# Performance work log

Measured on AMD Instinct MI355X. Metric: run time of the kernel, lower is better.

## Reference

```python
import jax, jax.numpy as jnp
import numpy as np

N_FEATURES = 64
KERNEL = 3
PAD = KERNEL // 2


def setup_inputs() -> dict:
    key = jax.random.key(0)
    ks = jax.random.split(key, 6)
    B, C, D, H, W = 2, N_FEATURES, 64, 64, 64
    Q = jax.random.normal(ks[0], (B, C, D, H, W), dtype=jnp.float32)
    K = jax.random.normal(ks[1], (B, C, D, H, W), dtype=jnp.float32)
    V = jax.random.normal(ks[2], (B, C, D, H, W), dtype=jnp.float32)
    # learned params: positional embedding (torch.randn init) and 1x1x1 conv
    pos_emb = jax.random.normal(ks[3], (C, KERNEL, KERNEL, KERNEL), dtype=jnp.float32)
    fan_in = C  # 1x1x1 conv fan-in
    bound = 1.0 / np.sqrt(fan_in)
    W_out = jax.random.uniform(ks[4], (C, C), minval=-bound, maxval=bound, dtype=jnp.float32)
    b_out = jax.random.uniform(ks[5], (C,), minval=-bound, maxval=bound, dtype=jnp.float32)
    return {"Q": Q, "K": K, "V": V, "pos_emb": pos_emb, "W_out": W_out, "b_out": b_out}


def reference(Q, K, V, pos_emb, W_out, b_out):
    B, C, D, H, W = Q.shape
    scale = 1.0 / np.sqrt(C).astype(np.float32)
    pad = ((0, 0), (0, 0), (PAD, PAD), (PAD, PAD), (PAD, PAD))
    Kp = jnp.pad(K, pad)
    Vp = jnp.pad(V, pad)
    # scores over the 27 kernel offsets (fixed small loop; data dims vectorized)
    scores = []
    for i in range(KERNEL):
        for j in range(KERNEL):
            for k in range(KERNEL):
                Ks = Kp[:, :, i:i + D, j:j + H, k:k + W]  # (B,C,D,H,W)
                pe = pos_emb[:, i, j, k][None, :, None, None, None]
                scores.append(jnp.sum(Q * (Ks + pe), axis=1) * scale)  # (B,D,H,W)
    attn = jax.nn.softmax(jnp.stack(scores, axis=1), axis=1)  # (B,27,D,H,W)
    x = jnp.zeros_like(Q)
    ijk = 0
    for i in range(KERNEL):
        for j in range(KERNEL):
            for k in range(KERNEL):
                Vs = Vp[:, :, i:i + D, j:j + H, k:k + W]
                x = x + attn[:, ijk][:, None] * Vs
                ijk += 1
    # 1x1x1 conv projection
    out = jnp.einsum('oc,bcdhw->bodhw', W_out, x) + b_out[None, :, None, None, None]
    return out
```

## Files before the change

### kernel.cpp

```cpp
#include <hip/hip_runtime.h>
#include <math.h>

#define CH 64
#define S 64
#define S2 (64 * 64)
#define S3 (64 * 64 * 64)

typedef short short8_t __attribute__((ext_vector_type(8)));
typedef float float4_t __attribute__((ext_vector_type(4)));

__device__ __align__(16) unsigned short WB_buf[CH * CH];
__device__ __align__(16) unsigned short peT_buf[32 * 64];

__device__ __forceinline__ unsigned short f2bf(float f) {
  unsigned int u = __float_as_uint(f);
  return (unsigned short)((u + 0x7FFFu + ((u >> 16) & 1u)) >> 16);
}

__global__ __launch_bounds__(256) void wprep(const float* __restrict__ W,
                                             const float* __restrict__ pe) {
  int i = blockIdx.x * 256 + threadIdx.x;
  if (i < 4096) {
    WB_buf[i] = f2bf(W[i]);
  } else {
    int j = i - 4096;
    int t = j >> 6, c = j & 63;
    peT_buf[t * 64 + c] = (t < 27) ? f2bf(pe[c * 27 + t]) : (unsigned short)0;
  }
}

__global__ __launch_bounds__(256) void attn_fused(const float* __restrict__ Q,
                                                  const float* __restrict__ K,
                                                  const float* __restrict__ V,
                                                  const float* __restrict__ bias,
                                                  float* __restrict__ out) {
  __shared__ unsigned short xs[4][CH][68];
  int tid = threadIdx.x;
  int lane = tid & 63;
  int wv = tid >> 6;

  int raw = blockIdx.x;
  int sw = (raw & 7) * 256 + (raw >> 3);
  int b = sw >> 10;
  int r = sw & 1023;
  int d = r >> 4;
  int hu = __builtin_amdgcn_readfirstlane((r & 15) * 4 + wv);

  size_t bbase = (size_t)b << 24;
  const float* Qb = Q + bbase;
  const float* Kb = K + bbase;
  const float* Vb = V + bbase;
  float* outb = out + bbase;

  float lmL = (lane == 0) ? 0.f : 1.f;
  float lmR = (lane == 63) ? 0.f : 1.f;

  int rowoff[9];
  float okf[9];
  const float* krow[9];
#pragma unroll
  for (int dz = 0; dz < 3; ++dz)
#pragma unroll
    for (int dy = 0; dy < 3; ++dy) {
      int rr = dz * 3 + dy;
      int zz = d + dz - 1, yy = hu + dy - 1;
      bool ok = ((unsigned)zz < 64u) & ((unsigned)yy < 64u);
      int zc = zz < 0 ? 0 : (zz > 63 ? 63 : zz);
      int yc = yy < 0 ? 0 : (yy > 63 ? 63 : yy);
      rowoff[rr] = __builtin_amdgcn_readfirstlane(zc * S2 + yc * S);
      krow[rr] = Kb + rowoff[rr];
      okf[rr] = ok ? 1.f : 0.f;
    }
  int upos = d * S2 + hu * S;
  int pos = upos + lane;

  float sC[9], sXR[9], sXL[9];
#pragma unroll
  for (int rr = 0; rr < 9; ++rr) { sC[rr] = 0.f; sXR[rr] = 0.f; sXL[rr] = 0.f; }

#pragma unroll 2
  for (int c2 = 0; c2 < CH; c2 += 2) {
    unsigned int qpack = 0;
#pragma unroll
    for (int u = 0; u < 2; ++u) {
      int coff = (c2 + u) * S3;
      float q = Qb[coff + pos];
      float rv[9];
#pragma unroll
      for (int rr = 0; rr < 9; ++rr) rv[rr] = krow[rr][coff + lane];
      float qR = __shfl_down(q, 1);
      float qL = __shfl_up(q, 1);
#pragma unroll
      for (int rr = 0; rr < 9; ++rr) {
        sC[rr]  = fmaf(q,  rv[rr], sC[rr]);
        sXR[rr] = fmaf(qR, rv[rr], sXR[rr]);
        sXL[rr] = fmaf(qL, rv[rr], sXL[rr]);
      }
      qpack |= ((unsigned int)f2bf(q)) << (16 * u);
    }
    *(unsigned int*)&xs[wv][lane][c2] = qpack;
  }

  __asm__ __volatile__("" ::: "memory");
  __threadfence_block();

  {
    int n16 = lane & 15, g = lane >> 4;
    short8_t pfr[4];
#pragma unroll
    for (int mt = 0; mt < 2; ++mt)
#pragma unroll
      for (int kc = 0; kc < 2; ++kc)
        pfr[mt * 2 + kc] =
            *(const short8_t*)(peT_buf + (mt * 16 + n16) * 64 + kc * 32 + g * 8);
    float* spf = (float*)&xs[wv][0][0];
#pragma unroll 1
    for (int nt = 0; nt < 4; ++nt) {
      const unsigned short* bp = &xs[wv][nt * 16 + n16][g * 8];
      union { short8_t v; uint2 h[2]; } u0, u1;
      u0.h[0] = *(const uint2*)(bp);
      u0.h[1] = *(const uint2*)(bp + 4);
      u1.h[0] = *(const uint2*)(bp + 32);
      u1.h[1] = *(const uint2*)(bp + 36);
#pragma unroll
      for (int mt = 0; mt < 2; ++mt) {
        float4_t acc = {0.f, 0.f, 0.f, 0.f};
        acc = __builtin_amdgcn_mfma_f32_16x16x32_bf16(pfr[mt * 2],     u0.v, acc, 0, 0, 0);
        acc = __builtin_amdgcn_mfma_f32_16x16x32_bf16(pfr[mt * 2 + 1], u1.v, acc, 0, 0, 0);
#pragma unroll
        for (int j = 0; j < 4; ++j)
          spf[(nt * 16 + n16) * 33 + mt * 16 + g * 4 + j] = acc[j];
      }
    }
  }

  __asm__ __volatile__("" ::: "memory");
  __threadfence_block();

  float s[27];
  {
    const float* spf = (const float*)&xs[wv][0][0];
    int sbase = lane * 33;
#pragma unroll
    for (int rr = 0; rr < 9; ++rr) {
      float lt = __shfl_up(sXR[rr], 1);
      float rt = __shfl_down(sXL[rr], 1);
      s[rr * 3]     = fmaf(lt * lmL, okf[rr], spf[sbase + rr * 3]);
      s[rr * 3 + 1] = fmaf(sC[rr],   okf[rr], spf[sbase + rr * 3 + 1]);
      s[rr * 3 + 2] = fmaf(rt * lmR, okf[rr], spf[sbase + rr * 3 + 2]);
    }
  }

  const float SC = 0.125f * 1.44269504088896f;
#pragma unroll
  for (int t = 0; t < 27; ++t) s[t] *= SC;
  float m = s[0];
#pragma unroll
  for (int t = 1; t < 27; ++t) m = fmaxf(m, s[t]);
  float sum = 0.f;
#pragma unroll
  for (int t = 0; t < 27; ++t) {
    s[t] = exp2f(s[t] - m);
    sum += s[t];
  }
  float inv = 1.f / sum;

  float wC[9], sLs[9], sRs[9];
  const float* vrow[9];
#pragma unroll
  for (int rr = 0; rr < 9; ++rr) {
    vrow[rr] = Vb + rowoff[rr];
    float f = inv * okf[rr];
    float wL = s[rr * 3] * f;
    wC[rr]   = s[rr * 3 + 1] * f;
    float wR = s[rr * 3 + 2] * f;
    sLs[rr] = __shfl_down(wL, 1);
    sRs[rr] = __shfl_up(wR, 1);
  }

  __asm__ __volatile__("" ::: "memory");
  __threadfence_block();

#pragma unroll 2
  for (int c2 = 0; c2 < CH; c2 += 2) {
    unsigned int packed = 0;
#pragma unroll
    for (int u = 0; u < 2; ++u) {
      int coff = (c2 + u) * S3;
      float rv[9];
#pragma unroll
      for (int rr = 0; rr < 9; ++rr) rv[rr] = vrow[rr][coff + lane];
      float own = 0.f, cR = 0.f, cL = 0.f;
#pragma unroll
      for (int rr = 0; rr < 9; ++rr) {
        own = fmaf(wC[rr], rv[rr], own);
        cR  = fmaf(sLs[rr], rv[rr], cR);
        cL  = fmaf(sRs[rr], rv[rr], cL);
      }
      float x_c = own + __shfl_up(cR, 1) * lmL + __shfl_down(cL, 1) * lmR;
      packed |= ((unsigned int)f2bf(x_c)) << (16 * u);
    }
    *(unsigned int*)&xs[wv][lane][c2] = packed;
  }

  __asm__ __volatile__("" ::: "memory");
  __threadfence_block();

  {
    int n16 = lane & 15, g = lane >> 4;
#pragma unroll 1
    for (int ot = 0; ot < 4; ++ot) {
      short8_t a0 = *(const short8_t*)(WB_buf + (ot * 16 + n16) * CH + g * 8);
      short8_t a1 = *(const short8_t*)(WB_buf + (ot * 16 + n16) * CH + 32 + g * 8);
      int obase = ot * 16 + 4 * g;
      float4_t bv = *(const float4_t*)(bias + obase);
#pragma unroll 1
      for (int pt = 0; pt < 4; ++pt) {
        const unsigned short* bp = &xs[wv][pt * 16 + n16][g * 8];
        union { short8_t v; uint2 h[2]; } u0, u1;
        u0.h[0] = *(const uint2*)(bp);
        u0.h[1] = *(const uint2*)(bp + 4);
        u1.h[0] = *(const uint2*)(bp + 32);
        u1.h[1] = *(const uint2*)(bp + 36);
        float4_t acc = {0.f, 0.f, 0.f, 0.f};
        acc = __builtin_amdgcn_mfma_f32_16x16x32_bf16(a0, u0.v, acc, 0, 0, 0);
        acc = __builtin_amdgcn_mfma_f32_16x16x32_bf16(a1, u1.v, acc, 0, 0, 0);
#pragma unroll
        for (int j = 0; j < 4; ++j)
          outb[(obase + j) * S3 + upos + pt * 16 + n16] = acc[j] + bv[j];
      }
    }
  }
}

extern "C" void kernel_launch(void* const* d_in, const int* in_sizes, int n_in,
                              void* d_out, int out_size, void* d_ws, size_t ws_size,
                              hipStream_t stream) {
  const float* Q = (const float*)d_in[0];
  const float* K = (const float*)d_in[1];
  const float* V = (const float*)d_in[2];
  const float* pe = (const float*)d_in[3];
  const float* W = (const float*)d_in[4];
  const float* bias = (const float*)d_in[5];
  float* out = (float*)d_out;

  wprep<<<24, 256, 0, stream>>>(W, pe);
  attn_fused<<<2048, 256, 0, stream>>>(Q, K, V, bias, out);
}
```

Measured before the change: 203.9 us.

## Process two voxels per lane with float2 loads and two rows per wave

Each wave now covers two H rows, with each lane owning two adjacent W positions. Q, K and V are read as float2 vectors, and the horizontal neighbour scores are computed in registers, so fewer cross-lane shuffles are needed. The grid is halved and shared memory per wave doubles to hold 128 positions. This amortises index math and issues fewer, wider loads, but it raises register pressure from about 54 score accumulators per lane, which may reduce occupancy.

```diff
diff --git a/kernel.cpp b/kernel.cpp
--- a/kernel.cpp
+++ b/kernel.cpp
@@ -34,17 +34,18 @@
                                                   const float* __restrict__ V,
                                                   const float* __restrict__ bias,
                                                   float* __restrict__ out) {
-  __shared__ unsigned short xs[4][CH][68];
+  __shared__ unsigned short xs[4][128][68];
   int tid = threadIdx.x;
   int lane = tid & 63;
   int wv = tid >> 6;
+  int wp = lane & 31, hoff = lane >> 5;
 
   int raw = blockIdx.x;
-  int sw = (raw & 7) * 256 + (raw >> 3);
-  int b = sw >> 10;
-  int r = sw & 1023;
-  int d = r >> 4;
-  int hu = __builtin_amdgcn_readfirstlane((r & 15) * 4 + wv);
+  int sw = (raw & 7) * 128 + (raw >> 3);
+  int b = sw >> 9;
+  int r = sw & 511;
+  int d = r >> 3;
+  int h0 = __builtin_amdgcn_readfirstlane(((r & 7) * 4 + wv) * 2);
 
   size_t bbase = (size_t)b << 24;
   const float* Qb = Q + bbase;
@@ -52,53 +53,61 @@
   const float* Vb = V + bbase;
   float* outb = out + bbase;
 
-  float lmL = (lane == 0) ? 0.f : 1.f;
-  float lmR = (lane == 63) ? 0.f : 1.f;
-
-  int rowoff[9];
+  int hl = h0 + hoff;
+  float lmL0 = (wp == 0) ? 0.f : 1.f;
+  float lmR1 = (wp == 31) ? 0.f : 1.f;
+
+  int offw[9];
   float okf[9];
-  const float* krow[9];
 #pragma unroll
   for (int dz = 0; dz < 3; ++dz)
 #pragma unroll
     for (int dy = 0; dy < 3; ++dy) {
       int rr = dz * 3 + dy;
-      int zz = d + dz - 1, yy = hu + dy - 1;
+      int zz = d + dz - 1, yy = hl + dy - 1;
       bool ok = ((unsigned)zz < 64u) & ((unsigned)yy < 64u);
       int zc = zz < 0 ? 0 : (zz > 63 ? 63 : zz);
       int yc = yy < 0 ? 0 : (yy > 63 ? 63 : yy);
-      rowoff[rr] = __builtin_amdgcn_readfirstlane(zc * S2 + yc * S);
-      krow[rr] = Kb + rowoff[rr];
+      offw[rr] = zc * S2 + yc * S + 2 * wp;
       okf[rr] = ok ? 1.f : 0.f;
     }
-  int upos = d * S2 + hu * S;
-  int pos = upos + lane;
-
-  float sC[9], sXR[9], sXL[9];
-#pragma unroll
-  for (int rr = 0; rr < 9; ++rr) { sC[rr] = 0.f; sXR[rr] = 0.f; sXL[rr] = 0.f; }
+  int qoff = d * S2 + hl * S + 2 * wp;
+  int p0 = hoff * 64 + 2 * wp, p1 = p0 + 1;
+
+  float s0C[9], s0R[9], s1L[9], s1C[9], a0Lp[9], s1Rp[9];
+#pragma unroll
+  for (int rr = 0; rr < 9; ++rr) {
+    s0C[rr] = 0.f; s0R[rr] = 0.f; s1L[rr] = 0.f;
+    s1C[rr] = 0.f; a0Lp[rr] = 0.f; s1Rp[rr] = 0.f;
+  }
 
 #pragma unroll 2
   for (int c2 = 0; c2 < CH; c2 += 2) {
-    unsigned int qpack = 0;
+    unsigned int qp0 = 0, qp1 = 0;
 #pragma unroll
     for (int u = 0; u < 2; ++u) {
       int coff = (c2 + u) * S3;
-      float q = Qb[coff + pos];
-      float rv[9];
-#pragma unroll
-      for (int rr = 0; rr < 9; ++rr) rv[rr] = krow[rr][coff + lane];
-      float qR = __shfl_down(q, 1);
-      float qL = __shfl_up(q, 1);
+      float2 qv = *(const float2*)(Qb + coff + qoff);
+      float2 kv[9];
+#pragma unroll
+      for (int rr = 0; rr < 9; ++rr)
+        kv[rr] = *(const float2*)(Kb + coff + offw[rr]);
+      float q0n = __shfl_down(qv.x, 1);
+      float q1p = __shfl_up(qv.y, 1);
 #pragma unroll
       for (int rr = 0; rr < 9; ++rr) {
-        sC[rr]  = fmaf(q,  rv[rr], sC[rr]);
-        sXR[rr] = fmaf(qR, rv[rr], sXR[rr]);
-        sXL[rr] = fmaf(qL, rv[rr], sXL[rr]);
-      }
-      qpack |= ((unsigned int)f2bf(q)) << (16 * u);
-    }
-    *(unsigned int*)&xs[wv][lane][c2] = qpack;
+        s0C[rr]  = fmaf(qv.x, kv[rr].x, s0C[rr]);
+        s0R[rr]  = fmaf(qv.x, kv[rr].y, s0R[rr]);
+        s1L[rr]  = fmaf(qv.y, kv[rr].x, s1L[rr]);
+        s1C[rr]  = fmaf(qv.y, kv[rr].y, s1C[rr]);
+        a0Lp[rr] = fmaf(q0n,  kv[rr].y, a0Lp[rr]);
+        s1Rp[rr] = fmaf(q1p,  kv[rr].x, s1Rp[rr]);
+      }
+      qp0 |= ((unsigned int)f2bf(qv.x)) << (16 * u);
+      qp1 |= ((unsigned int)f2bf(qv.y)) << (16 * u);
+    }
+    *(unsigned int*)&xs[wv][p0][c2] = qp0;
+    *(unsigned int*)&xs[wv][p1][c2] = qp1;
   }
 
   __asm__ __volatile__("" ::: "memory");
@@ -115,7 +124,7 @@
             *(const short8_t*)(peT_buf + (mt * 16 + n16) * 64 + kc * 32 + g * 8);
     float* spf = (float*)&xs[wv][0][0];
 #pragma unroll 1
-    for (int nt = 0; nt < 4; ++nt) {
+    for (int nt = 0; nt < 8; ++nt) {
       const unsigned short* bp = &xs[wv][nt * 16 + n16][g * 8];
       union { short8_t v; uint2 h[2]; } u0, u1;
       u0.h[0] = *(const uint2*)(bp);
@@ -137,45 +146,47 @@
   __asm__ __volatile__("" ::: "memory");
   __threadfence_block();
 
-  float s[27];
+  float s0[27], s1[27];
   {
     const float* spf = (const float*)&xs[wv][0][0];
-    int sbase = lane * 33;
+    int b0 = p0 * 33, b1 = p1 * 33;
 #pragma unroll
     for (int rr = 0; rr < 9; ++rr) {
-      float lt = __shfl_up(sXR[rr], 1);
-      float rt = __shfl_down(sXL[rr], 1);
-      s[rr * 3]     = fmaf(lt * lmL, okf[rr], spf[sbase + rr * 3]);
-      s[rr * 3 + 1] = fmaf(sC[rr],   okf[rr], spf[sbase + rr * 3 + 1]);
-      s[rr * 3 + 2] = fmaf(rt * lmR, okf[rr], spf[sbase + rr * 3 + 2]);
+      float l0 = __shfl_up(a0Lp[rr], 1) * lmL0;
+      float r1 = __shfl_down(s1Rp[rr], 1) * lmR1;
+      s0[rr * 3]     = fmaf(l0,      okf[rr], spf[b0 + rr * 3]);
+      s0[rr * 3 + 1] = fmaf(s0C[rr], okf[rr], spf[b0 + rr * 3 + 1]);
+      s0[rr * 3 + 2] = fmaf(s0R[rr], okf[rr], spf[b0 + rr * 3 + 2]);
+      s1[rr * 3]     = fmaf(s1L[rr], okf[rr], spf[b1 + rr * 3]);
+      s1[rr * 3 + 1] = fmaf(s1C[rr], okf[rr], spf[b1 + rr * 3 + 1]);
+      s1[rr * 3 + 2] = fmaf(r1,      okf[rr], spf[b1 + rr * 3 + 2]);
     }
   }
 
   const float SC = 0.125f * 1.44269504088896f;
 #pragma unroll
-  for (int t = 0; t < 27; ++t) s[t] *= SC;
-  float m = s[0];
-#pragma unroll
-  for (int t = 1; t < 27; ++t) m = fmaxf(m, s[t]);
-  float sum = 0.f;
+  for (int t = 0; t < 27; ++t) { s0[t] *= SC; s1[t] *= SC; }
+  float m0 = s0[0], m1 = s1[0];
+#pragma unroll
+  for (int t = 1; t < 27; ++t) { m0 = fmaxf(m0, s0[t]); m1 = fmaxf(m1, s1[t]); }
+  float sum0 = 0.f, sum1 = 0.f;
 #pragma unroll
   for (int t = 0; t < 27; ++t) {
-    s[t] = exp2f(s[t] - m);
-    sum += s[t];
-  }
-  float inv = 1.f / sum;
-
-  float wC[9], sLs[9], sRs[9];
-  const float* vrow[9];
+    s0[t] = exp2f(s0[t] - m0); sum0 += s0[t];
+    s1[t] = exp2f(s1[t] - m1); sum1 += s1[t];
+  }
+  float inv0 = 1.f / sum0, inv1 = 1.f / sum1;
+
+  float wC0[9], wR0[9], wL1[9], wC1[9], sL0s[9], sR1s[9];
 #pragma unroll
   for (int rr = 0; rr < 9; ++rr) {
-    vrow[rr] = Vb + rowoff[rr];
-    float f = inv * okf[rr];
-    float wL = s[rr * 3] * f;
-    wC[rr]   = s[rr * 3 + 1] * f;
-    float wR = s[rr * 3 + 2] * f;
-    sLs[rr] = __shfl_down(wL, 1);
-    sRs[rr] = __shfl_up(wR, 1);
+    float f0 = inv0 * okf[rr], f1 = inv1 * okf[rr];
+    wC0[rr] = s0[rr * 3 + 1] * f0;
+    wR0[rr] = s0[rr * 3 + 2] * f0;
+    wL1[rr] = s1[rr * 3] * f1;
+    wC1[rr] = s1[rr * 3 + 1] * f1;
+    sL0s[rr] = __shfl_down(s0[rr * 3] * f0, 1);
+    sR1s[rr] = __shfl_up(s1[rr * 3 + 2] * f1, 1);
   }
 
   __asm__ __volatile__("" ::: "memory");
@@ -183,24 +194,31 @@
 
 #pragma unroll 2
   for (int c2 = 0; c2 < CH; c2 += 2) {
-    unsigned int packed = 0;
+    unsigned int xp0 = 0, xp1 = 0;
 #pragma unroll
     for (int u = 0; u < 2; ++u) {
       int coff = (c2 + u) * S3;
-      float rv[9];
-#pragma unroll
-      for (int rr = 0; rr < 9; ++rr) rv[rr] = vrow[rr][coff + lane];
-      float own = 0.f, cR = 0.f, cL = 0.f;
+      float2 vv[9];
+#pragma unroll
+      for (int rr = 0; rr < 9; ++rr)
+        vv[rr] = *(const float2*)(Vb + coff + offw[rr]);
+      float own0 = 0.f, own1 = 0.f, cX0 = 0.f, cX1 = 0.f;
 #pragma unroll
       for (int rr = 0; rr < 9; ++rr) {
-        own = fmaf(wC[rr], rv[rr], own);
-        cR  = fmaf(sLs[rr], rv[rr], cR);
-        cL  = fmaf(sRs[rr], rv[rr], cL);
-      }
-      float x_c = own + __shfl_up(cR, 1) * lmL + __shfl_down(cL, 1) * lmR;
-      packed |= ((unsigned int)f2bf(x_c)) << (16 * u);
-    }
-    *(unsigned int*)&xs[wv][lane][c2] = packed;
+        own0 = fmaf(wC0[rr], vv[rr].x, own0);
+        own0 = fmaf(wR0[rr], vv[rr].y, own0);
+        own1 = fmaf(wL1[rr], vv[rr].x, own1);
+        own1 = fmaf(wC1[rr], vv[rr].y, own1);
+        cX0  = fmaf(sL0s[rr], vv[rr].y, cX0);
+        cX1  = fmaf(sR1s[rr], vv[rr].x, cX1);
+      }
+      float x0 = own0 + __shfl_up(cX0, 1) * lmL0;
+      float x1 = own1 + __shfl_down(cX1, 1) * lmR1;
+      xp0 |= ((unsigned int)f2bf(x0)) << (16 * u);
+      xp1 |= ((unsigned int)f2bf(x1)) << (16 * u);
+    }
+    *(unsigned int*)&xs[wv][p0][c2] = xp0;
+    *(unsigned int*)&xs[wv][p1][c2] = xp1;
   }
 
   __asm__ __volatile__("" ::: "memory");
@@ -208,6 +226,7 @@
 
   {
     int n16 = lane & 15, g = lane >> 4;
+    int upos0 = d * S2 + h0 * S;
 #pragma unroll 1
     for (int ot = 0; ot < 4; ++ot) {
       short8_t a0 = *(const short8_t*)(WB_buf + (ot * 16 + n16) * CH + g * 8);
@@ -215,7 +234,7 @@
       int obase = ot * 16 + 4 * g;
       float4_t bv = *(const float4_t*)(bias + obase);
 #pragma unroll 1
-      for (int pt = 0; pt < 4; ++pt) {
+      for (int pt = 0; pt < 8; ++pt) {
         const unsigned short* bp = &xs[wv][pt * 16 + n16][g * 8];
         union { short8_t v; uint2 h[2]; } u0, u1;
         u0.h[0] = *(const uint2*)(bp);
@@ -225,9 +244,10 @@
         float4_t acc = {0.f, 0.f, 0.f, 0.f};
         acc = __builtin_amdgcn_mfma_f32_16x16x32_bf16(a0, u0.v, acc, 0, 0, 0);
         acc = __builtin_amdgcn_mfma_f32_16x16x32_bf16(a1, u1.v, acc, 0, 0, 0);
+        int pidx = upos0 + (pt >> 2) * S + (pt & 3) * 16 + n16;
 #pragma unroll
         for (int j = 0; j < 4; ++j)
-          outb[(obase + j) * S3 + upos + pt * 16 + n16] = acc[j] + bv[j];
+          outb[(obase + j) * S3 + pidx] = acc[j] + bv[j];
       }
     }
   }
@@ -245,5 +265,5 @@
   float* out = (float*)d_out;
 
   wprep<<<24, 256, 0, stream>>>(W, pe);
-  attn_fused<<<2048, 256, 0, stream>>>(Q, K, V, bias, out);
-}
+  attn_fused<<<1024, 256, 0, stream>>>(Q, K, V, bias, out);
+}
```

Result: slower. 236.3 us (+15.9%).
